# Performance work log

Hardware: AMD Instinct MI355X
Metric: run time of the kernel (lower is better)

Reference implementation:

```python
import jax, jax.numpy as jnp
import numpy as np

# Multi-scale feature pyramid (static: determines per-level slice bounds)
SPATIAL_SHAPES = np.array([[100, 100], [50, 50], [25, 25], [13, 13], [7, 7]])  # (H, W) per level
LEVEL_START = np.concatenate([[0], np.cumsum(SPATIAL_SHAPES[:, 0] * SPATIAL_SHAPES[:, 1])])[:-1]
C = 256       # hidden_inplanes
HEADS = 8     # head_nums
POINTS = 4    # point_nums
LEVELS = 5    # feature_level_nums
FF = 2048     # feedforward_planes
DH = C // HEADS


def setup_inputs() -> dict:
    key = jax.random.key(0)
    ks = jax.random.split(key, 16)
    B = 2
    L = int((SPATIAL_SHAPES[:, 0] * SPATIAL_SHAPES[:, 1]).sum())  # 13343 tokens
    s = 0.02
    return {
        'src': jax.random.normal(ks[0], (B, L, C), jnp.float32),
        'pos': jax.random.normal(ks[1], (B, L, C), jnp.float32) * 0.1,
        'reference_points': jax.random.uniform(ks[2], (B, L, LEVELS, 2), jnp.float32),
        'wv': jax.random.normal(ks[3], (C, C), jnp.float32) * s,
        'bv': jnp.zeros((C,), jnp.float32),
        'wo': jax.random.normal(ks[4], (C, HEADS * LEVELS * POINTS * 2), jnp.float32) * s,
        'bo': jax.random.normal(ks[5], (HEADS * LEVELS * POINTS * 2,), jnp.float32) * 0.5,
        'wa': jax.random.normal(ks[6], (C, HEADS * LEVELS * POINTS), jnp.float32) * s,
        'ba': jnp.zeros((HEADS * LEVELS * POINTS,), jnp.float32),
        'wout': jax.random.normal(ks[7], (C, C), jnp.float32) * s,
        'bout': jnp.zeros((C,), jnp.float32),
        'ln1g': jnp.ones((C,), jnp.float32),
        'ln1b': jnp.zeros((C,), jnp.float32),
        'w1': jax.random.normal(ks[8], (C, FF), jnp.float32) * s,
        'b1': jnp.zeros((FF,), jnp.float32),
        'w2': jax.random.normal(ks[9], (FF, C), jnp.float32) * s,
        'b2': jnp.zeros((C,), jnp.float32),
        'ln2g': jnp.ones((C,), jnp.float32),
        'ln2b': jnp.zeros((C,), jnp.float32),
    }


def layernorm(x, g, b, eps=1e-5):
    m = jnp.mean(x, -1, keepdims=True)
    v = jnp.var(x, -1, keepdims=True)
    return (x - m) * jax.lax.rsqrt(v + eps) * g + b


def bilinear_sample(val, loc, Hs, Ws):
    # val: [B, heads, H*W, dh]   loc: [B, heads, Lq, P, 2] normalized coords in [0,1]
    # grid_sample semantics, align_corners=False, zero padding outside
    px = loc[..., 0] * Ws - 0.5
    py = loc[..., 1] * Hs - 0.5
    x0 = jnp.floor(px); y0 = jnp.floor(py)
    lx = px - x0;       ly = py - y0
    x0i = x0.astype(jnp.int32); y0i = y0.astype(jnp.int32)
    gather = jax.vmap(jax.vmap(lambda v, i: v[i]))  # over batch, head dims
    out = jnp.zeros(loc.shape[:-1] + (val.shape[-1],), val.dtype)
    for dx, dy, w in ((0, 0, (1 - lx) * (1 - ly)), (1, 0, lx * (1 - ly)),
                      (0, 1, (1 - lx) * ly), (1, 1, lx * ly)):
        xi = x0i + dx; yi = y0i + dy
        valid = (xi >= 0) & (xi < Ws) & (yi >= 0) & (yi < Hs)
        idx = jnp.clip(yi, 0, Hs - 1) * Ws + jnp.clip(xi, 0, Ws - 1)
        g = gather(val, idx)  # [B, heads, Lq, P, dh]
        out = out + (w * valid)[..., None] * g
    return out


def msdeform_attn(query, value_in, ref, wv, bv, wo, bo, wa, ba, wout, bout):
    B, Lq, _ = query.shape
    # value projection -> [B, heads, Len, dh]
    value = (value_in @ wv + bv).reshape(B, -1, HEADS, DH).transpose(0, 2, 1, 3)
    offsets = (query @ wo + bo).reshape(B, Lq, HEADS, LEVELS, POINTS, 2)
    attn = jax.nn.softmax((query @ wa + ba).reshape(B, Lq, HEADS, LEVELS * POINTS), -1)
    attn = attn.reshape(B, Lq, HEADS, LEVELS, POINTS)
    # offset normalizer = (W, H) per level
    norml = jnp.asarray(SPATIAL_SHAPES[:, ::-1].copy(), jnp.float32)
    loc = ref[:, :, None, :, None, :] + offsets / norml[None, None, None, :, None, :]
    acc = jnp.zeros((B, Lq, HEADS, DH), query.dtype)
    for l in range(LEVELS):
        Hs, Ws = int(SPATIAL_SHAPES[l, 0]), int(SPATIAL_SHAPES[l, 1])
        s = int(LEVEL_START[l])
        vl = value[:, :, s:s + Hs * Ws, :]
        locl = jnp.transpose(loc[:, :, :, l], (0, 2, 1, 3, 4))  # [B, heads, Lq, P, 2]
        samp = bilinear_sample(vl, locl, Hs, Ws)                 # [B, heads, Lq, P, dh]
        acc = acc + jnp.einsum('bhqpd,bqhp->bqhd', samp, attn[:, :, :, l])
    return acc.reshape(B, Lq, C) @ wout + bout


def reference(src, pos, reference_points, wv, bv, wo, bo, wa, ba, wout, bout,
              ln1g, ln1b, w1, b1, w2, b2, ln2g, ln2b):
    # DeformableTransformerEncoderLayer (eval mode, dropout off)
    q = src + pos
    src2 = msdeform_attn(q, src, reference_points, wv, bv, wo, bo, wa, ba, wout, bout)
    x = layernorm(src + src2, ln1g, ln1b)
    ffn = jax.nn.relu(x @ w1 + b1) @ w2 + b2
    return layernorm(x + ffn, ln2g, ln2b)
```

## Files before the change

kernel.cpp:

```cpp
#include <hip/hip_runtime.h>
#include <hip/hip_bf16.h>
#include <hip/hip_fp16.h>

typedef __hip_bfloat16 bf16;
typedef unsigned short ushort_t;
typedef __attribute__((ext_vector_type(8))) short bf16x8;
typedef __attribute__((ext_vector_type(16))) float f32x16;

__device__ __forceinline__ float us2f(unsigned short u) {
    unsigned int x = ((unsigned int)u) << 16;
    return __uint_as_float(x);
}
__device__ __forceinline__ ushort_t f2us(float f) {
    return ((__hip_bfloat16_raw)__float2bfloat16(f)).x;
}

__device__ __forceinline__ void gl_lds16(const ushort_t* g, ushort_t* l) {
    __builtin_amdgcn_global_load_lds(
        (const __attribute__((address_space(1))) void*)g,
        (__attribute__((address_space(3))) void*)l, 16, 0, 0);
}

__global__ __launch_bounds__(256) void cast2_kernel(
    const float* __restrict__ src, const float* __restrict__ pos,
    bf16* __restrict__ src_b, bf16* __restrict__ q_b, int n)
{
    int i = (blockIdx.x * 256 + threadIdx.x) * 4;
    if (i < n) {
        const float4 s4 = *reinterpret_cast<const float4*>(&src[i]);
        const float4 p4 = *reinterpret_cast<const float4*>(&pos[i]);
        int2 sp, qp;
        sp.x = (unsigned)f2us(s4.x) | ((unsigned)f2us(s4.y) << 16);
        sp.y = (unsigned)f2us(s4.z) | ((unsigned)f2us(s4.w) << 16);
        qp.x = (unsigned)f2us(s4.x + p4.x) | ((unsigned)f2us(s4.y + p4.y) << 16);
        qp.y = (unsigned)f2us(s4.z + p4.z) | ((unsigned)f2us(s4.w + p4.w) << 16);
        *reinterpret_cast<int2*>((ushort_t*)src_b + i) = sp;
        *reinterpret_cast<int2*>((ushort_t*)q_b + i) = qp;
    }
}

__global__ __launch_bounds__(256) void prep_kernel(
    const float* __restrict__ wv, const float* __restrict__ wo,
    const float* __restrict__ wa, const float* __restrict__ wout,
    const float* __restrict__ w1, const float* __restrict__ w2,
    const float* __restrict__ bo, const float* __restrict__ ba,
    bf16* __restrict__ wvt, bf16* __restrict__ wcat, bf16* __restrict__ woutt,
    ushort_t* __restrict__ w1p, ushort_t* __restrict__ w2p,
    float* __restrict__ bcat)
{
    __shared__ float tile[32][33];
    const int b = blockIdx.x;
    const float* W; bf16* Wt = nullptr; ushort_t* Wp = nullptr;
    int K, N, tb, mode = 0;
    if (b < 64)        { W = wv;   Wt = wvt;            K = 256;  N = 256;  tb = b; }
    else if (b < 144)  { W = wo;   Wt = wcat;           K = 256;  N = 320;  tb = b - 64; }
    else if (b < 184)  { W = wa;   Wt = wcat + 320*256; K = 256;  N = 160;  tb = b - 144; }
    else if (b < 248)  { W = wout; Wt = woutt;          K = 256;  N = 256;  tb = b - 184; }
    else if (b < 760)  { W = w1;   Wp = w1p; mode = 1;  K = 256;  N = 2048; tb = b - 248; }
    else if (b < 1272) { W = w2;   Wp = w2p; mode = 2;  K = 2048; N = 256;  tb = b - 760; }
    else {
        int i = (b - 1272) * 256 + threadIdx.x;
        if (i < 320) bcat[i] = bo[i];
        else if (i < 480) bcat[i] = ba[i - 320];
        return;
    }
    const int ntn = N >> 5;
    const int nb = (tb % ntn) * 32, kb = (tb / ntn) * 32;
    const int tx = threadIdx.x & 31, ty = threadIdx.x >> 5;
    #pragma unroll
    for (int i = 0; i < 32; i += 8) {
        int k = kb + ty + i, n = nb + tx;
        tile[ty + i][tx] = (k < K && n < N) ? W[(size_t)k * N + n] : 0.f;
    }
    __syncthreads();
    if (mode == 0) {
        #pragma unroll
        for (int i = 0; i < 32; i += 8) {
            int n = nb + ty + i, k = kb + tx;
            if (n < N && k < K)
                Wt[(size_t)n * K + k] = __float2bfloat16(tile[tx][ty + i]);
        }
    } else if (threadIdx.x < 128) {
        const int l = threadIdx.x & 63, kw = threadIdx.x >> 6;
        const int kb8 = kw * 16 + (l >> 5) * 8;
        const int nx = l & 31;
        ushort_t tmp[8];
        #pragma unroll
        for (int e = 0; e < 8; ++e) tmp[e] = f2us(tile[kb8 + e][nx]);
        size_t base;
        if (mode == 1)
            base = ((size_t)(((nb >> 5) * 8 + (kb >> 5)) * 2 + kw)) * 512;
        else
            base = ((size_t)((((kb >> 7) * 8 + (nb >> 5)) * 4 + ((kb >> 5) & 3)) * 2 + kw)) * 512;
        *reinterpret_cast<int4*>(Wp + base + l * 8) =
            *reinterpret_cast<const int4*>(tmp);
    }
}

template<bool RELU, bool OUT_BF16, bool HAS_RESID, bool RESID_BF16, int NT, int WPE>
__global__ __launch_bounds__(256, WPE) void gemm_mfma_s(
    const ushort_t* __restrict__ A,
    const ushort_t* __restrict__ Bt,
    const float* __restrict__ bias,
    const void* __restrict__ residv,
    void* __restrict__ outv, int M, int N, int K, int mtiles)
{
    __shared__ __align__(16) char smemraw[24576];
    ushort_t* Asmem = (ushort_t*)smemraw;
    ushort_t* Bsmem = (ushort_t*)(smemraw + 4096);
    float (*epi)[68] = (float(*)[68])smemraw;

    const int lid = blockIdx.x;
    const int tbk = lid >> 3;
    const int xb = tbk & (NT - 1);
    const int yg = (tbk / NT) * 8 + (lid & 7);
    if (yg >= mtiles) return;
    const int m0 = yg * 64;
    const int n0 = xb * 128;

    const int tid = threadIdx.x;
    const int lane = tid & 63;
    const int wave = tid >> 6;
    const int l32 = lane & 31;
    const int hi  = lane >> 5;
    const int wm = wave >> 1;
    const int wn = wave & 1;

    const int lsup = lane >> 3;
    const int clin = lane & 7;

    const int gsA = wave * 8 + lsup;
    const int csA = clin ^ (gsA & 7);
    int rA = m0 + gsA * 2 + (csA >> 2); if (rA > M - 1) rA = M - 1;
    const ushort_t* aP = A + (size_t)rA * K + (csA & 3) * 8;
    ushort_t* aL = Asmem + wave * 512;

    const ushort_t* bP[2]; ushort_t* bL[2];
    #pragma unroll
    for (int i = 0; i < 2; ++i) {
        const int gsB = wave * 16 + i * 8 + lsup;
        const int csB = clin ^ (gsB & 7);
        int rB = n0 + gsB * 2 + (csB >> 2); if (rB > N - 1) rB = N - 1;
        bP[i] = Bt + (size_t)rB * K + (csB & 3) * 8;
        bL[i] = Bsmem + (wave * 16 + i * 8) * 64;
    }

    const int arow = wm * 32 + l32;
    const int asup = arow >> 1;
    const ushort_t* aR[2];
    #pragma unroll
    for (int kw = 0; kw < 2; ++kw) {
        const int q = kw * 2 + hi;
        const int slot = (((arow & 1) << 2) | q) ^ (asup & 7);
        aR[kw] = Asmem + asup * 64 + slot * 8;
    }
    const ushort_t* bR[2][2];
    #pragma unroll
    for (int j = 0; j < 2; ++j) {
        const int brow = wn * 64 + j * 32 + l32;
        const int bsup = brow >> 1;
        #pragma unroll
        for (int kw = 0; kw < 2; ++kw) {
            const int q = kw * 2 + hi;
            const int slot = (((brow & 1) << 2) | q) ^ (bsup & 7);
            bR[j][kw] = Bsmem + bsup * 64 + slot * 8;
        }
    }

    f32x16 acc[2] = {};

    auto stage = [&](int ofs) {
        gl_lds16(aP, aL + ofs);             aP    += 32;
        gl_lds16(bP[0], bL[0] + ofs);       bP[0] += 32;
        gl_lds16(bP[1], bL[1] + ofs);       bP[1] += 32;
    };
    auto compute = [&](int ofs) {
        #pragma unroll
        for (int kw = 0; kw < 2; ++kw) {
            const bf16x8 af = *reinterpret_cast<const bf16x8*>(aR[kw] + ofs);
            #pragma unroll
            for (int j = 0; j < 2; ++j)
                acc[j] = __builtin_amdgcn_mfma_f32_32x32x16_bf16(
                    af, *reinterpret_cast<const bf16x8*>(bR[j][kw] + ofs),
                    acc[j], 0, 0, 0);
        }
    };

    const int ntile = K >> 5;
    stage(0);
    for (int t = 0; t < ntile; t += 2) {
        __syncthreads();
        stage(6144);
        compute(0);
        __syncthreads();
        if (t + 2 < ntile) stage(0);
        compute(6144);
    }
    __syncthreads();

    #pragma unroll
    for (int half = 0; half < 2; ++half) {
        if (wn == half) {
            #pragma unroll
            for (int j = 0; j < 2; ++j) {
                const int coll = j * 32 + l32;
                const int n = n0 + half * 64 + coll;
                const float bv = (n < N) ? bias[n] : 0.f;
                #pragma unroll
                for (int r = 0; r < 16; ++r) {
                    const int row = wm * 32 + hi * 4 + (r & 3) + (r >> 2) * 8;
                    epi[row][coll] = acc[j][r] + bv;
                }
            }
        }
        __syncthreads();
        #pragma unroll
        for (int i = 0; i < 4; ++i) {
            const int idx = i * 256 + tid;
            const int row = idx >> 4;
            const int c4  = idx & 15;
            const int m = m0 + row;
            const int n = n0 + half * 64 + c4 * 4;
            if (m < M && n + 3 < N) {
                float4 v = *reinterpret_cast<const float4*>(&epi[row][c4 * 4]);
                if (HAS_RESID) {
                    if (RESID_BF16) {
                        const int2 rw = *reinterpret_cast<const int2*>(
                            (const ushort_t*)residv + (size_t)m * N + n);
                        v.x += us2f((ushort_t)((unsigned)rw.x & 0xffffu));
                        v.y += us2f((ushort_t)((unsigned)rw.x >> 16));
                        v.z += us2f((ushort_t)((unsigned)rw.y & 0xffffu));
                        v.w += us2f((ushort_t)((unsigned)rw.y >> 16));
                    } else {
                        const float4 r4 = *reinterpret_cast<const float4*>(
                            (const float*)residv + (size_t)m * N + n);
                        v.x += r4.x; v.y += r4.y; v.z += r4.z; v.w += r4.w;
                    }
                }
                if (RELU) {
                    v.x = fmaxf(v.x, 0.f); v.y = fmaxf(v.y, 0.f);
                    v.z = fmaxf(v.z, 0.f); v.w = fmaxf(v.w, 0.f);
                }
                if (OUT_BF16) {
                    int2 pk;
                    pk.x = (unsigned)f2us(v.x) | ((unsigned)f2us(v.y) << 16);
                    pk.y = (unsigned)f2us(v.z) | ((unsigned)f2us(v.w) << 16);
                    *reinterpret_cast<int2*>((ushort_t*)outv + (size_t)m * N + n) = pk;
                } else {
                    *reinterpret_cast<float4*>((float*)outv + (size_t)m * N + n) = v;
                }
            }
        }
        if (half == 0) __syncthreads();
    }
}

template<bool RELU, bool OUT_BF16, bool HAS_RESID, bool RESID_BF16, int NT>
__global__ __launch_bounds__(256, 4) void gemm_mfma_b(
    const ushort_t* __restrict__ A,
    const ushort_t* __restrict__ Bt,
    const float* __restrict__ bias,
    const void* __restrict__ residv,
    void* __restrict__ outv, int M, int N, int K, int mtiles)
{
    __shared__ __align__(16) char smemraw[32768];
    ushort_t* Asmem = (ushort_t*)smemraw;
    ushort_t* Bsmem = (ushort_t*)(smemraw + 8192);
    float (*epi)[68] = (float(*)[68])smemraw;

    const int lid = blockIdx.x;
    const int tbk = lid >> 3;
    const int xb = tbk & (NT - 1);
    const int yg = (tbk / NT) * 8 + (lid & 7);
    if (yg >= mtiles) return;
    const int m0 = yg * 128;
    const int n0 = xb * 128;

    const int tid = threadIdx.x;
    const int lane = tid & 63;
    const int wave = tid >> 6;
    const int l32 = lane & 31;
    const int hi  = lane >> 5;
    const int wm = wave >> 1;
    const int wn = wave & 1;

    const int lsup = lane >> 3;
    const int clin = lane & 7;
    const ushort_t *aP[2], *bP[2];
    ushort_t *aL[2], *bL[2];
    #pragma unroll
    for (int i = 0; i < 2; ++i) {
        const int gs = wave * 16 + i * 8 + lsup;
        const int cs = clin ^ (gs & 7);
        int rA = m0 + gs * 2 + (cs >> 2); if (rA > M - 1) rA = M - 1;
        aP[i] = A + (size_t)rA * K + (cs & 3) * 8;
        aL[i] = Asmem + (wave * 16 + i * 8) * 64;
        int rB = n0 + gs * 2 + (cs >> 2); if (rB > N - 1) rB = N - 1;
        bP[i] = Bt + (size_t)rB * K + (cs & 3) * 8;
        bL[i] = Bsmem + (wave * 16 + i * 8) * 64;
    }

    const ushort_t* aR[2][2];
    const ushort_t* bR[2][2];
    #pragma unroll
    for (int mi = 0; mi < 2; ++mi) {
        const int arow = wm * 64 + mi * 32 + l32;
        const int asup = arow >> 1;
        #pragma unroll
        for (int kw = 0; kw < 2; ++kw) {
            const int q = kw * 2 + hi;
            const int slot = (((arow & 1) << 2) | q) ^ (asup & 7);
            aR[mi][kw] = Asmem + asup * 64 + slot * 8;
        }
    }
    #pragma unroll
    for (int ni = 0; ni < 2; ++ni) {
        const int brow = wn * 64 + ni * 32 + l32;
        const int bsup = brow >> 1;
        #pragma unroll
        for (int kw = 0; kw < 2; ++kw) {
            const int q = kw * 2 + hi;
            const int slot = (((brow & 1) << 2) | q) ^ (bsup & 7);
            bR[ni][kw] = Bsmem + bsup * 64 + slot * 8;
        }
    }

    f32x16 a00 = {}, a01 = {}, a10 = {}, a11 = {};

    auto stage = [&](int ofs) {
        gl_lds16(aP[0], aL[0] + ofs); aP[0] += 32;
        gl_lds16(aP[1], aL[1] + ofs); aP[1] += 32;
        gl_lds16(bP[0], bL[0] + ofs); bP[0] += 32;
        gl_lds16(bP[1], bL[1] + ofs); bP[1] += 32;
    };
    auto compute = [&](int ofs) {
        #pragma unroll
        for (int kw = 0; kw < 2; ++kw) {
            const bf16x8 af0 = *reinterpret_cast<const bf16x8*>(aR[0][kw] + ofs);
            const bf16x8 af1 = *reinterpret_cast<const bf16x8*>(aR[1][kw] + ofs);
            const bf16x8 bf0 = *reinterpret_cast<const bf16x8*>(bR[0][kw] + ofs);
            const bf16x8 bf1 = *reinterpret_cast<const bf16x8*>(bR[1][kw] + ofs);
            a00 = __builtin_amdgcn_mfma_f32_32x32x16_bf16(af0, bf0, a00, 0, 0, 0);
            a01 = __builtin_amdgcn_mfma_f32_32x32x16_bf16(af0, bf1, a01, 0, 0, 0);
            a10 = __builtin_amdgcn_mfma_f32_32x32x16_bf16(af1, bf0, a10, 0, 0, 0);
            a11 = __builtin_amdgcn_mfma_f32_32x32x16_bf16(af1, bf1, a11, 0, 0, 0);
        }
    };

    const int ntile = K >> 5;
    stage(0);
    for (int t = 0; t < ntile; t += 2) {
        __syncthreads();
        stage(8192);
        compute(0);
        __syncthreads();
        if (t + 2 < ntile) stage(0);
        compute(8192);
    }
    __syncthreads();

    #pragma unroll
    for (int qd = 0; qd < 4; ++qd) {
        const int rh = qd >> 1, ch = qd & 1;
        if (qd) __syncthreads();
        if (wm == rh && wn == ch) {
            #pragma unroll
            for (int ni = 0; ni < 2; ++ni) {
                const int col = ni * 32 + l32;
                const int n = n0 + ch * 64 + col;
                const float bv = (n < N) ? bias[n] : 0.f;
                #pragma unroll
                for (int mi = 0; mi < 2; ++mi) {
                    const f32x16& ac = (mi == 0) ? (ni == 0 ? a00 : a01)
                                                 : (ni == 0 ? a10 : a11);
                    #pragma unroll
                    for (int r = 0; r < 16; ++r) {
                        const int row = mi * 32 + hi * 4 + (r & 3) + (r >> 2) * 8;
                        epi[row][col] = ac[r] + bv;
                    }
                }
            }
        }
        __syncthreads();
        #pragma unroll
        for (int i = 0; i < 4; ++i) {
            const int idx = i * 256 + tid;
            const int row = idx >> 4;
            const int c4  = idx & 15;
            const int m = m0 + rh * 64 + row;
            const int n = n0 + ch * 64 + c4 * 4;
            if (m < M && n + 3 < N) {
                float4 v = *reinterpret_cast<const float4*>(&epi[row][c4 * 4]);
                if (HAS_RESID) {
                    if (RESID_BF16) {
                        const int2 rw = *reinterpret_cast<const int2*>(
                            (const ushort_t*)residv + (size_t)m * N + n);
                        v.x += us2f((ushort_t)((unsigned)rw.x & 0xffffu));
                        v.y += us2f((ushort_t)((unsigned)rw.x >> 16));
                        v.z += us2f((ushort_t)((unsigned)rw.y & 0xffffu));
                        v.w += us2f((ushort_t)((unsigned)rw.y >> 16));
                    } else {
                        const float4 r4 = *reinterpret_cast<const float4*>(
                            (const float*)residv + (size_t)m * N + n);
                        v.x += r4.x; v.y += r4.y; v.z += r4.z; v.w += r4.w;
                    }
                }
                if (RELU) {
                    v.x = fmaxf(v.x, 0.f); v.y = fmaxf(v.y, 0.f);
                    v.z = fmaxf(v.z, 0.f); v.w = fmaxf(v.w, 0.f);
                }
                if (OUT_BF16) {
                    int2 pk;
                    pk.x = (unsigned)f2us(v.x) | ((unsigned)f2us(v.y) << 16);
                    pk.y = (unsigned)f2us(v.z) | ((unsigned)f2us(v.w) << 16);
                    *reinterpret_cast<int2*>((ushort_t*)outv + (size_t)m * N + n) = pk;
                } else {
                    *reinterpret_cast<float4*>((float*)outv + (size_t)m * N + n) = v;
                }
            }
        }
    }
}

__global__ __launch_bounds__(256, 3) void ffn_fused2(
    const ushort_t* __restrict__ X,
    const ushort_t* __restrict__ W1p,
    const ushort_t* __restrict__ W2p,
    const float* __restrict__ b1, const float* __restrict__ b2,
    const float* __restrict__ g, const float* __restrict__ beta,
    float* __restrict__ out, int M)
{
    __shared__ __align__(16) char smem[33280];
    ushort_t* Xs = (ushort_t*)smem;
    ushort_t* Hs = (ushort_t*)(smem + 16384);
    float (*epi)[260] = (float(*)[260])smem;

    const int m0 = blockIdx.x * 32;
    const int tid = threadIdx.x;
    const int lane = tid & 63;
    const int wave = tid >> 6;
    const int l32 = lane & 31;
    const int hi  = lane >> 5;

    {
        const int lsup = (wave & 1) * 8 + (lane >> 3);
        const int clin = lane & 7;
        const int cs = clin ^ (lsup & 7);
        int r = m0 + lsup * 2 + (cs >> 2); if (r > M - 1) r = M - 1;
        const ushort_t* xp = X + (size_t)r * 256 + (cs & 3) * 8;
        ushort_t* xl = Xs + (wave & 1) * 512;
        #pragma unroll
        for (int p = 0; p < 4; ++p) {
            const int t = p * 2 + (wave >> 1);
            gl_lds16(xp + t * 32, xl + t * 1024);
        }
    }

    int aOff[2];
    {
        const int sr = l32 >> 1;
        #pragma unroll
        for (int kw = 0; kw < 2; ++kw) {
            const int q = kw * 2 + hi;
            const int slot = (((l32 & 1) << 2) | q) ^ (sr & 7);
            aOff[kw] = sr * 64 + slot * 8;
        }
    }
    int hadr[16];
    #pragma unroll
    for (int r = 0; r < 16; ++r) {
        const int m = (r & 3) + 8 * (r >> 2) + 4 * hi;
        const int slot = (((m & 1) << 2) | (l32 >> 3)) ^ ((m >> 1) & 7);
        hadr[r] = wave * 1024 + (m >> 1) * 64 + slot * 8 + (l32 & 7);
    }

    f32x16 za0 = {}, za1 = {};
    __syncthreads();

    for (int c = 0; c < 16; ++c) {
        f32x16 h0 = {}, h1 = {};
        const int hcg = c * 4 + wave;
        const ushort_t* w1c = W1p + (size_t)hcg * 8192;
        #pragma unroll
        for (int t = 0; t < 8; t += 2) {
            #pragma unroll
            for (int kw = 0; kw < 2; ++kw) {
                const bf16x8 a0 = *reinterpret_cast<const bf16x8*>(
                    Xs + t * 1024 + aOff[kw]);
                const bf16x8 a1 = *reinterpret_cast<const bf16x8*>(
                    Xs + (t + 1) * 1024 + aOff[kw]);
                const bf16x8 b0 = *reinterpret_cast<const bf16x8*>(
                    w1c + (t * 2 + kw) * 512 + lane * 8);
                const bf16x8 b1f = *reinterpret_cast<const bf16x8*>(
                    w1c + ((t + 1) * 2 + kw) * 512 + lane * 8);
                h0 = __builtin_amdgcn_mfma_f32_32x32x16_bf16(a0, b0, h0, 0, 0, 0);
                h1 = __builtin_amdgcn_mfma_f32_32x32x16_bf16(a1, b1f, h1, 0, 0, 0);
            }
        }
        const float bb = b1[hcg * 32 + l32];

        __syncthreads();
        #pragma unroll
        for (int r = 0; r < 16; ++r)
            Hs[hadr[r]] = f2us(fmaxf(h0[r] + h1[r] + bb, 0.f));
        __syncthreads();

        const ushort_t* w2c = W2p + (size_t)c * 32768;
        const int nq0 = wave * 2;
        #pragma unroll
        for (int t = 0; t < 4; ++t) {
            #pragma unroll
            for (int kw = 0; kw < 2; ++kw) {
                const bf16x8 af = *reinterpret_cast<const bf16x8*>(
                    Hs + t * 1024 + aOff[kw]);
                const bf16x8 bf0 = *reinterpret_cast<const bf16x8*>(
                    w2c + ((nq0 * 4 + t) * 2 + kw) * 512 + lane * 8);
                const bf16x8 bf1 = *reinterpret_cast<const bf16x8*>(
                    w2c + (((nq0 + 1) * 4 + t) * 2 + kw) * 512 + lane * 8);
                za0 = __builtin_amdgcn_mfma_f32_32x32x16_bf16(af, bf0, za0, 0, 0, 0);
                za1 = __builtin_amdgcn_mfma_f32_32x32x16_bf16(af, bf1, za1, 0, 0, 0);
            }
        }
    }

    __syncthreads();

    #pragma unroll
    for (int j = 0; j < 2; ++j) {
        const int col = wave * 64 + j * 32 + l32;
        const float bz = b2[col];
        const f32x16& zz = j ? za1 : za0;
        #pragma unroll
        for (int r = 0; r < 16; ++r)
            epi[(r & 3) + 8 * (r >> 2) + 4 * hi][col] = zz[r] + bz;
    }
    __syncthreads();

    const int row = tid >> 3, t8 = tid & 7;
    const int m = m0 + row;
    const int mc = (m < M) ? m : (M - 1);
    const ushort_t* xr = X + (size_t)mc * 256 + t8 * 32;
    float v[32];
    float s = 0.f, ss = 0.f;
    #pragma unroll
    for (int i = 0; i < 8; ++i) {
        const float4 e = *reinterpret_cast<const float4*>(
            &epi[row][t8 * 32 + i * 4]);
        const int2 rb = *reinterpret_cast<const int2*>(xr + i * 4);
        const float f0 = e.x + us2f((ushort_t)((unsigned)rb.x & 0xffffu));
        const float f1 = e.y + us2f((ushort_t)((unsigned)rb.x >> 16));
        const float f2 = e.z + us2f((ushort_t)((unsigned)rb.y & 0xffffu));
        const float f3 = e.w + us2f((ushort_t)((unsigned)rb.y >> 16));
        v[i * 4]     = f0; v[i * 4 + 1] = f1;
        v[i * 4 + 2] = f2; v[i * 4 + 3] = f3;
        s  += f0 + f1 + f2 + f3;
        ss += f0 * f0 + f1 * f1 + f2 * f2 + f3 * f3;
    }
    s += __shfl_xor(s, 1); ss += __shfl_xor(ss, 1);
    s += __shfl_xor(s, 2); ss += __shfl_xor(ss, 2);
    s += __shfl_xor(s, 4); ss += __shfl_xor(ss, 4);
    const float mean = s * (1.f / 256.f);
    const float var = ss * (1.f / 256.f) - mean * mean;
    const float rs = rsqrtf(var + 1e-5f);
    if (m < M) {
        #pragma unroll
        for (int i = 0; i < 8; ++i) {
            const float4 g4 = *reinterpret_cast<const float4*>(
                &g[t8 * 32 + i * 4]);
            const float4 b4 = *reinterpret_cast<const float4*>(
                &beta[t8 * 32 + i * 4]);
            float4 o4;
            o4.x = (v[i * 4]     - mean) * rs * g4.x + b4.x;
            o4.y = (v[i * 4 + 1] - mean) * rs * g4.y + b4.y;
            o4.z = (v[i * 4 + 2] - mean) * rs * g4.z + b4.z;
            o4.w = (v[i * 4 + 3] - mean) * rs * g4.w + b4.w;
            *reinterpret_cast<float4*>(
                &out[(size_t)m * 256 + t8 * 32 + i * 4]) = o4;
        }
    }
}

__global__ __launch_bounds__(256) void msda_kernel_v7(
    const ushort_t* __restrict__ og,
    const float* __restrict__ refp,
    const ushort_t* __restrict__ value,
    bf16* __restrict__ out,
    int M, int L)
{
    const int tid = threadIdx.x;
    const int nb = gridDim.x;
    int wk = blockIdx.x;
    if ((nb & 7) == 0) {
        const int per = nb >> 3;
        wk = (blockIdx.x & 7) * per + (blockIdx.x >> 3);
    }
    const int qbase = wk * 8;

    __shared__ float s_attn[8][160];
    __shared__ int2  s_off[1280];
    __shared__ int2  s_wh[1280];

    for (int i = tid; i < 1280; i += 256) {
        int q = i / 160, j = i - q * 160;
        int qq = qbase + q;
        s_attn[q][j] = (qq < M) ? us2f(og[(size_t)qq * 480 + 320 + j]) : 0.f;
    }
    __syncthreads();

    if (tid < 64) {
        float* a = &s_attn[tid >> 3][(tid & 7) * 20];
        float mx = -1e30f;
        #pragma unroll
        for (int i = 0; i < 20; ++i) mx = fmaxf(mx, a[i]);
        float ssum = 0.f;
        #pragma unroll
        for (int i = 0; i < 20; ++i) {
            float e = __expf(a[i] - mx);
            a[i] = e;
            ssum += e;
        }
        float inv = 1.f / ssum;
        #pragma unroll
        for (int i = 0; i < 20; ++i) a[i] *= inv;
    }
    __syncthreads();

    #pragma unroll
    for (int it = 0; it < 5; ++it) {
        const int t = tid + it * 256;
        const int q  = t / 160;
        const int r  = t - q * 160;
        const int l  = (r - (r / 20) * 20) >> 2;
        const int qq = qbase + q;

        int2 offp = {0, 0};
        __half2 h01 = __floats2half2_rn(0.f, 0.f);
        __half2 h23 = h01;
        if (qq < M) {
            const int Wi = (l == 0) ? 100 : (l == 1) ? 50 : (l == 2) ? 25
                         : (l == 3) ? 13 : 7;
            const int s0 = (l == 0) ? 0 : (l == 1) ? 10000 : (l == 2) ? 12500
                         : (l == 3) ? 13125 : 13294;
            const float Wf = (float)Wi;
            const float ox = us2f(og[(size_t)qq * 480 + r * 2]);
            const float oy = us2f(og[(size_t)qq * 480 + r * 2 + 1]);
            const float2 rf = *reinterpret_cast<const float2*>(
                &refp[(size_t)qq * 10 + l * 2]);
            const float a = s_attn[q][r];

            const float px = fmaf(rf.x, Wf, -0.5f) + ox;
            const float py = fmaf(rf.y, Wf, -0.5f) + oy;
            const float x0f = floorf(px);
            const float y0f = floorf(py);
            const float lx = px - x0f;
            const float ly = py - y0f;
            const int x0 = (int)x0f;
            const int y0 = (int)y0f;

            const float wx0v = (x0 >= 0 && x0 < Wi) ? (1.f - lx) : 0.f;
            const float wx1v = (x0 + 1 >= 0 && x0 + 1 < Wi) ? lx : 0.f;
            const float wy0v = (y0 >= 0 && y0 < Wi) ? (1.f - ly) : 0.f;
            const float wy1v = (y0 + 1 >= 0 && y0 + 1 < Wi) ? ly : 0.f;

            const int c0 = min(max(x0, 0), Wi - 2);
            const int r0 = min(max(y0, 0), Wi - 2);
            const float swx0 = (x0 == c0 ? wx0v : 0.f) + (x0 + 1 == c0 ? wx1v : 0.f);
            const float swx1 = (x0 == c0 + 1 ? wx0v : 0.f) + (x0 + 1 == c0 + 1 ? wx1v : 0.f);
            const float swy0 = (y0 == r0 ? wy0v : 0.f) + (y0 + 1 == r0 ? wy1v : 0.f);
            const float swy1 = (y0 == r0 + 1 ? wy0v : 0.f) + (y0 + 1 == r0 + 1 ? wy1v : 0.f);

            offp.x = (s0 + r0 * Wi + c0) * 512;
            offp.y = offp.x + Wi * 512;
            h01 = __floats2half2_rn(a * swx0 * swy0, a * swx1 * swy0);
            h23 = __floats2half2_rn(a * swx0 * swy1, a * swx1 * swy1);
        }
        s_off[t] = offp;
        union { __half2 h; int i; } c0u, c1u;
        c0u.h = h01; c1u.h = h23;
        int2 wpk; wpk.x = c0u.i; wpk.y = c1u.i;
        s_wh[t] = wpk;
    }
    __syncthreads();

    const int qi  = tid >> 5;
    const int g   = tid & 31;
    const int h   = g >> 2;
    const int sub = g & 3;
    const int bq = qbase + qi;
    if (bq >= M) return;
    const int b = bq / L;

    const char* vb = (const char*)value + (size_t)b * L * 512 + h * 64 + sub * 16;

    float acc[8] = {};
    const int tb = qi * 160 + h * 20;
    #pragma unroll 2
    for (int p = 0; p < 20; ++p) {
        const int2 off = s_off[tb + p];
        const int2 whp = s_wh[tb + p];
        const int4 u00 = *reinterpret_cast<const int4*>(vb + off.x);
        const int4 u10 = *reinterpret_cast<const int4*>(vb + off.x + 512);
        const int4 u01 = *reinterpret_cast<const int4*>(vb + off.y);
        const int4 u11 = *reinterpret_cast<const int4*>(vb + off.y + 512);
        union { int i; __half2 h; } w0u, w1u;
        w0u.i = whp.x; w1u.i = whp.y;
        const float2 w01 = __half22float2(w0u.h);
        const float2 w23 = __half22float2(w1u.h);
        #define ACC4(u, wt)                                                        \
            acc[0] = fmaf(wt, __uint_as_float((unsigned)(u).x << 16), acc[0]);      \
            acc[1] = fmaf(wt, __uint_as_float((unsigned)(u).x & 0xffff0000u), acc[1]); \
            acc[2] = fmaf(wt, __uint_as_float((unsigned)(u).y << 16), acc[2]);      \
            acc[3] = fmaf(wt, __uint_as_float((unsigned)(u).y & 0xffff0000u), acc[3]); \
            acc[4] = fmaf(wt, __uint_as_float((unsigned)(u).z << 16), acc[4]);      \
            acc[5] = fmaf(wt, __uint_as_float((unsigned)(u).z & 0xffff0000u), acc[5]); \
            acc[6] = fmaf(wt, __uint_as_float((unsigned)(u).w << 16), acc[6]);      \
            acc[7] = fmaf(wt, __uint_as_float((unsigned)(u).w & 0xffff0000u), acc[7]);
        ACC4(u00, w01.x)
        ACC4(u10, w01.y)
        ACC4(u01, w23.x)
        ACC4(u11, w23.y)
        #undef ACC4
    }

    ushort_t o[8];
    #pragma unroll
    for (int i = 0; i < 8; ++i) o[i] = f2us(acc[i]);
    int4 pkt;
    pkt.x = (int)o[0] | ((int)o[1] << 16);
    pkt.y = (int)o[2] | ((int)o[3] << 16);
    pkt.z = (int)o[4] | ((int)o[5] << 16);
    pkt.w = (int)o[6] | ((int)o[7] << 16);
    *reinterpret_cast<int4*>((ushort_t*)out + (size_t)bq * 256 + h * 32 + sub * 8) = pkt;
}

template<bool OUT_BF16>
__global__ __launch_bounds__(256) void ln_kernel(
    const ushort_t* __restrict__ yb, const float* __restrict__ g,
    const float* __restrict__ bta, void* __restrict__ outv, int M)
{
    const int wave = threadIdx.x >> 6, lane = threadIdx.x & 63;
    const int row = blockIdx.x * 4 + wave;
    if (row >= M) return;
    const int2 raw = *reinterpret_cast<const int2*>(&yb[(size_t)row * 256 + lane * 4]);
    float v0 = us2f((ushort_t)((unsigned)raw.x & 0xffffu));
    float v1 = us2f((ushort_t)((unsigned)raw.x >> 16));
    float v2 = us2f((ushort_t)((unsigned)raw.y & 0xffffu));
    float v3 = us2f((ushort_t)((unsigned)raw.y >> 16));
    float s  = v0 + v1 + v2 + v3;
    float ss = v0 * v0 + v1 * v1 + v2 * v2 + v3 * v3;
    #pragma unroll
    for (int o = 32; o > 0; o >>= 1) {
        s += __shfl_down(s, o);
        ss += __shfl_down(ss, o);
    }
    s = __shfl(s, 0);
    ss = __shfl(ss, 0);
    const float mean = s * (1.f / 256.f);
    const float var = ss * (1.f / 256.f) - mean * mean;
    const float rs = rsqrtf(var + 1e-5f);
    const float4 g4 = *reinterpret_cast<const float4*>(&g[lane * 4]);
    const float4 b4 = *reinterpret_cast<const float4*>(&bta[lane * 4]);
    float4 o4;
    o4.x = (v0 - mean) * rs * g4.x + b4.x;
    o4.y = (v1 - mean) * rs * g4.y + b4.y;
    o4.z = (v2 - mean) * rs * g4.z + b4.z;
    o4.w = (v3 - mean) * rs * g4.w + b4.w;
    if (OUT_BF16) {
        int2 pk;
        pk.x = (unsigned)f2us(o4.x) | ((unsigned)f2us(o4.y) << 16);
        pk.y = (unsigned)f2us(o4.z) | ((unsigned)f2us(o4.w) << 16);
        *reinterpret_cast<int2*>((ushort_t*)outv + (size_t)row * 256 + lane * 4) = pk;
    } else {
        *reinterpret_cast<float4*>((float*)outv + (size_t)row * 256 + lane * 4) = o4;
    }
}

extern "C" void kernel_launch(void* const* d_in, const int* in_sizes, int n_in,
                              void* d_out, int out_size, void* d_ws, size_t ws_size,
                              hipStream_t stream)
{
    const int B = 2, L = 13343, C = 256;
    const int M = B * L;

    const float* src  = (const float*)d_in[0];
    const float* pos  = (const float*)d_in[1];
    const float* refp = (const float*)d_in[2];
    const float* wv   = (const float*)d_in[3];
    const float* bv   = (const float*)d_in[4];
    const float* wo   = (const float*)d_in[5];
    const float* bo   = (const float*)d_in[6];
    const float* wa   = (const float*)d_in[7];
    const float* ba   = (const float*)d_in[8];
    const float* wout = (const float*)d_in[9];
    const float* bout = (const float*)d_in[10];
    const float* ln1g = (const float*)d_in[11];
    const float* ln1b = (const float*)d_in[12];
    const float* w1   = (const float*)d_in[13];
    const float* b1   = (const float*)d_in[14];
    const float* w2   = (const float*)d_in[15];
    const float* b2   = (const float*)d_in[16];
    const float* ln2g = (const float*)d_in[17];
    const float* ln2b = (const float*)d_in[18];

    char* ws = (char*)d_ws;
    const size_t MB = 1ull << 20;
    bf16*  src_b  = (bf16*)(ws + 0);
    bf16*  q_b    = (bf16*)(ws + 14 * MB);
    bf16*  val_b  = (bf16*)(ws + 28 * MB);
    bf16*  og     = (bf16*)(ws + 42 * MB);
    bf16*  acc_b  = (bf16*)(ws + 95 * MB);
    bf16*  y      = (bf16*)(ws + 110 * MB);
    bf16*  x_b    = (bf16*)(ws + 138 * MB);
    bf16* wvt    = (bf16*)(ws + 152 * MB);
    bf16* wcat   = wvt + 256 * 256;
    bf16* woutt  = wcat + 480 * 256;
    ushort_t* w1p = (ushort_t*)(woutt + 256 * 256);
    ushort_t* w2p = w1p + 2048 * 256;
    float* bcat  = (float*)(w2p + 256 * 2048);
    (void)ws_size; (void)n_in; (void)in_sizes; (void)out_size;

    const int mt64  = (M + 63) / 64;
    const int gm8   = (mt64 + 7) / 8;
    const int mt128 = (M + 127) / 128;
    const int gb8   = (mt128 + 7) / 8;
    const int mt32  = (M + 31) / 32;
    const int lnb   = (M + 3) / 4;

    prep_kernel<<<1274, 256, 0, stream>>>(wv, wo, wa, wout, w1, w2, bo, ba,
                                          wvt, wcat, woutt, w1p, w2p, bcat);

    cast2_kernel<<<(M * C / 4 + 255) / 256, 256, 0, stream>>>(
        src, pos, src_b, q_b, M * C);

    gemm_mfma_s<false, true, false, false, 2, 4><<<gm8 * 16, 256, 0, stream>>>(
        (const ushort_t*)src_b, (const ushort_t*)wvt, bv, nullptr, val_b,
        M, 256, 256, mt64);

    gemm_mfma_b<false, true, false, false, 4><<<gb8 * 32, 256, 0, stream>>>(
        (const ushort_t*)q_b, (const ushort_t*)wcat, bcat, nullptr, og,
        M, 480, 256, mt128);

    msda_kernel_v7<<<(M + 7) / 8, 256, 0, stream>>>(
        (const ushort_t*)og, refp, (const ushort_t*)val_b, acc_b, M, L);

    gemm_mfma_s<false, true, true, false, 2, 4><<<gm8 * 16, 256, 0, stream>>>(
        (const ushort_t*)acc_b, (const ushort_t*)woutt, bout, src, y,
        M, 256, 256, mt64);

    ln_kernel<true><<<lnb, 256, 0, stream>>>(
        (const ushort_t*)y, ln1g, ln1b, x_b, M);

    ffn_fused2<<<mt32, 256, 0, stream>>>(
        (const ushort_t*)x_b, w1p, w2p, b1, b2, ln2g, ln2b,
        (float*)d_out, M);
}
```

Before: 352.6 us.

## Keep FFN hidden tile in registers and split second GEMM over K across waves

The fused FFN kernel now computes the first GEMM transposed (weights as the A operand), so the ReLU'd hidden chunk lands in registers in the layout needed as the A operand of the second GEMM. Lanes exchange halves with a cross-lane shuffle instead of writing the chunk to shared memory. This removes two block barriers and an LDS round trip per chunk. Each wave then accumulates all 8 output column tiles over its own slice of K, and the partial sums are reduced through shared memory in a staggered four-phase epilogue. The cost is 128 accumulator registers per thread, which lowers the occupancy bound from 3 to 2 blocks, plus extra epilogue barriers.

Result: slower. 466.0 us (+32.2%).

```diff
diff --git a/kernel.cpp b/kernel.cpp
--- a/kernel.cpp
+++ b/kernel.cpp
@@ -422,7 +422,7 @@
     }
 }
 
-__global__ __launch_bounds__(256, 3) void ffn_fused2(
+__global__ __launch_bounds__(256, 2) void ffn_fused3(
     const ushort_t* __restrict__ X,
     const ushort_t* __restrict__ W1p,
     const ushort_t* __restrict__ W2p,
@@ -432,7 +432,6 @@
 {
     __shared__ __align__(16) char smem[33280];
     ushort_t* Xs = (ushort_t*)smem;
-    ushort_t* Hs = (ushort_t*)(smem + 16384);
     float (*epi)[260] = (float(*)[260])smem;
 
     const int m0 = blockIdx.x * 32;
@@ -441,6 +440,7 @@
     const int wave = tid >> 6;
     const int l32 = lane & 31;
     const int hi  = lane >> 5;
+    const bool hb = (hi != 0);
 
     {
         const int lsup = (wave & 1) * 8 + (lane >> 3);
@@ -466,15 +466,8 @@
             aOff[kw] = sr * 64 + slot * 8;
         }
     }
-    int hadr[16];
-    #pragma unroll
-    for (int r = 0; r < 16; ++r) {
-        const int m = (r & 3) + 8 * (r >> 2) + 4 * hi;
-        const int slot = (((m & 1) << 2) | (l32 >> 3)) ^ ((m >> 1) & 7);
-        hadr[r] = wave * 1024 + (m >> 1) * 64 + slot * 8 + (l32 & 7);
-    }
-
-    f32x16 za0 = {}, za1 = {};
+
+    f32x16 za[8] = {};
     __syncthreads();
 
     for (int c = 0; c < 16; ++c) {
@@ -485,56 +478,79 @@
         for (int t = 0; t < 8; t += 2) {
             #pragma unroll
             for (int kw = 0; kw < 2; ++kw) {
-                const bf16x8 a0 = *reinterpret_cast<const bf16x8*>(
+                const bf16x8 xa0 = *reinterpret_cast<const bf16x8*>(
                     Xs + t * 1024 + aOff[kw]);
-                const bf16x8 a1 = *reinterpret_cast<const bf16x8*>(
+                const bf16x8 xa1 = *reinterpret_cast<const bf16x8*>(
                     Xs + (t + 1) * 1024 + aOff[kw]);
-                const bf16x8 b0 = *reinterpret_cast<const bf16x8*>(
+                const bf16x8 wA0 = *reinterpret_cast<const bf16x8*>(
                     w1c + (t * 2 + kw) * 512 + lane * 8);
-                const bf16x8 b1f = *reinterpret_cast<const bf16x8*>(
+                const bf16x8 wA1 = *reinterpret_cast<const bf16x8*>(
                     w1c + ((t + 1) * 2 + kw) * 512 + lane * 8);
-                h0 = __builtin_amdgcn_mfma_f32_32x32x16_bf16(a0, b0, h0, 0, 0, 0);
-                h1 = __builtin_amdgcn_mfma_f32_32x32x16_bf16(a1, b1f, h1, 0, 0, 0);
+                h0 = __builtin_amdgcn_mfma_f32_32x32x16_bf16(wA0, xa0, h0, 0, 0, 0);
+                h1 = __builtin_amdgcn_mfma_f32_32x32x16_bf16(wA1, xa1, h1, 0, 0, 0);
             }
         }
-        const float bb = b1[hcg * 32 + l32];
-
+
+        float4 bq[4];
+        #pragma unroll
+        for (int p = 0; p < 4; ++p)
+            bq[p] = *reinterpret_cast<const float4*>(b1 + hcg * 32 + p * 8 + 4 * hi);
+        int pk[8];
+        #pragma unroll
+        for (int i = 0; i < 8; ++i) {
+            const int p = i >> 1;
+            const float bv0 = (i & 1) ? bq[p].z : bq[p].x;
+            const float bv1 = (i & 1) ? bq[p].w : bq[p].y;
+            const float v0 = fmaxf(h0[2 * i]     + h1[2 * i]     + bv0, 0.f);
+            const float v1 = fmaxf(h0[2 * i + 1] + h1[2 * i + 1] + bv1, 0.f);
+            pk[i] = (int)((unsigned)f2us(v0) | ((unsigned)f2us(v1) << 16));
+        }
+        int sw[8];
+        #pragma unroll
+        for (int i = 0; i < 8; ++i) sw[i] = __shfl_xor(pk[i], 32);
+
+        union { int4 i4; bf16x8 v; } uf0, uf1;
+        uf0.i4.x = hb ? sw[2] : pk[0];
+        uf0.i4.y = hb ? sw[3] : pk[1];
+        uf0.i4.z = hb ? pk[2] : sw[0];
+        uf0.i4.w = hb ? pk[3] : sw[1];
+        uf1.i4.x = hb ? sw[6] : pk[4];
+        uf1.i4.y = hb ? sw[7] : pk[5];
+        uf1.i4.z = hb ? pk[6] : sw[4];
+        uf1.i4.w = hb ? pk[7] : sw[5];
+
+        const ushort_t* w2c = W2p + (size_t)c * 32768;
+        #pragma unroll
+        for (int nq = 0; nq < 8; ++nq) {
+            const bf16x8 wb0 = *reinterpret_cast<const bf16x8*>(
+                w2c + ((nq * 4 + wave) * 2 + 0) * 512 + lane * 8);
+            const bf16x8 wb1 = *reinterpret_cast<const bf16x8*>(
+                w2c + ((nq * 4 + wave) * 2 + 1) * 512 + lane * 8);
+            za[nq] = __builtin_amdgcn_mfma_f32_32x32x16_bf16(uf0.v, wb0, za[nq], 0, 0, 0);
+            za[nq] = __builtin_amdgcn_mfma_f32_32x32x16_bf16(uf1.v, wb1, za[nq], 0, 0, 0);
+        }
+    }
+
+    __syncthreads();
+
+    #pragma unroll
+    for (int q = 0; q < 4; ++q) {
+        const int cg = (wave + q) & 3;
+        #pragma unroll
+        for (int nq = 0; nq < 8; ++nq) {
+            if ((nq >> 1) == cg) {
+                const int col = nq * 32 + l32;
+                #pragma unroll
+                for (int r = 0; r < 16; ++r) {
+                    const int row = (r & 3) + 8 * (r >> 2) + 4 * hi;
+                    float v = za[nq][r];
+                    if (q) v += epi[row][col];
+                    epi[row][col] = v;
+                }
+            }
+        }
         __syncthreads();
-        #pragma unroll
-        for (int r = 0; r < 16; ++r)
-            Hs[hadr[r]] = f2us(fmaxf(h0[r] + h1[r] + bb, 0.f));
-        __syncthreads();
-
-        const ushort_t* w2c = W2p + (size_t)c * 32768;
-        const int nq0 = wave * 2;
-        #pragma unroll
-        for (int t = 0; t < 4; ++t) {
-            #pragma unroll
-            for (int kw = 0; kw < 2; ++kw) {
-                const bf16x8 af = *reinterpret_cast<const bf16x8*>(
-                    Hs + t * 1024 + aOff[kw]);
-                const bf16x8 bf0 = *reinterpret_cast<const bf16x8*>(
-                    w2c + ((nq0 * 4 + t) * 2 + kw) * 512 + lane * 8);
-                const bf16x8 bf1 = *reinterpret_cast<const bf16x8*>(
-                    w2c + (((nq0 + 1) * 4 + t) * 2 + kw) * 512 + lane * 8);
-                za0 = __builtin_amdgcn_mfma_f32_32x32x16_bf16(af, bf0, za0, 0, 0, 0);
-                za1 = __builtin_amdgcn_mfma_f32_32x32x16_bf16(af, bf1, za1, 0, 0, 0);
-            }
-        }
-    }
-
-    __syncthreads();
-
-    #pragma unroll
-    for (int j = 0; j < 2; ++j) {
-        const int col = wave * 64 + j * 32 + l32;
-        const float bz = b2[col];
-        const f32x16& zz = j ? za1 : za0;
-        #pragma unroll
-        for (int r = 0; r < 16; ++r)
-            epi[(r & 3) + 8 * (r >> 2) + 4 * hi][col] = zz[r] + bz;
-    }
-    __syncthreads();
+    }
 
     const int row = tid >> 3, t8 = tid & 7;
     const int m = m0 + row;
@@ -546,11 +562,13 @@
     for (int i = 0; i < 8; ++i) {
         const float4 e = *reinterpret_cast<const float4*>(
             &epi[row][t8 * 32 + i * 4]);
+        const float4 bz = *reinterpret_cast<const float4*>(
+            &b2[t8 * 32 + i * 4]);
         const int2 rb = *reinterpret_cast<const int2*>(xr + i * 4);
-        const float f0 = e.x + us2f((ushort_t)((unsigned)rb.x & 0xffffu));
-        const float f1 = e.y + us2f((ushort_t)((unsigned)rb.x >> 16));
-        const float f2 = e.z + us2f((ushort_t)((unsigned)rb.y & 0xffffu));
-        const float f3 = e.w + us2f((ushort_t)((unsigned)rb.y >> 16));
+        const float f0 = e.x + bz.x + us2f((ushort_t)((unsigned)rb.x & 0xffffu));
+        const float f1 = e.y + bz.y + us2f((ushort_t)((unsigned)rb.x >> 16));
+        const float f2 = e.z + bz.z + us2f((ushort_t)((unsigned)rb.y & 0xffffu));
+        const float f3 = e.w + bz.w + us2f((ushort_t)((unsigned)rb.y >> 16));
         v[i * 4]     = f0; v[i * 4 + 1] = f1;
         v[i * 4 + 2] = f2; v[i * 4 + 3] = f3;
         s  += f0 + f1 + f2 + f3;
@@ -850,7 +868,7 @@
     ln_kernel<true><<<lnb, 256, 0, stream>>>(
         (const ushort_t*)y, ln1g, ln1b, x_b, M);
 
-    ffn_fused2<<<mt32, 256, 0, stream>>>(
+    ffn_fused3<<<mt32, 256, 0, stream>>>(
         (const ushort_t*)x_b, w1p, w2p, b1, b2, ln2g, ln2b,
         (float*)d_out, M);
 }
```

## Fuse output projection, residual add and first LayerNorm into one kernel

Applied to the files above, without the earlier changes.

Replaces the separate wout GEMM (which wrote a bf16 intermediate y) and the standalone LayerNorm kernel with a single kernel. Each block computes 32 rows of the projection with MFMA, using the same pre-packed weight layout as the FFN kernel, then adds bias and the fp32 residual and applies LayerNorm in an LDS epilogue. This removes one launch and the write and re-read of the intermediate. In exchange, weight fragments are read straight from global memory for every 32-row block, and the residual is now added in fp32 before rounding.

Result: no change. 355.5 us (+0.8%).

```diff
diff --git a/kernel.cpp b/kernel.cpp
--- a/kernel.cpp
+++ b/kernel.cpp
@@ -44,7 +44,8 @@
     const float* __restrict__ wa, const float* __restrict__ wout,
     const float* __restrict__ w1, const float* __restrict__ w2,
     const float* __restrict__ bo, const float* __restrict__ ba,
-    bf16* __restrict__ wvt, bf16* __restrict__ wcat, bf16* __restrict__ woutt,
+    bf16* __restrict__ wvt, bf16* __restrict__ wcat,
+    ushort_t* __restrict__ woutp,
     ushort_t* __restrict__ w1p, ushort_t* __restrict__ w2p,
     float* __restrict__ bcat)
 {
@@ -55,7 +56,7 @@
     if (b < 64)        { W = wv;   Wt = wvt;            K = 256;  N = 256;  tb = b; }
     else if (b < 144)  { W = wo;   Wt = wcat;           K = 256;  N = 320;  tb = b - 64; }
     else if (b < 184)  { W = wa;   Wt = wcat + 320*256; K = 256;  N = 160;  tb = b - 144; }
-    else if (b < 248)  { W = wout; Wt = woutt;          K = 256;  N = 256;  tb = b - 184; }
+    else if (b < 248)  { W = wout; Wp = woutp; mode = 1; K = 256; N = 256;  tb = b - 184; }
     else if (b < 760)  { W = w1;   Wp = w1p; mode = 1;  K = 256;  N = 2048; tb = b - 248; }
     else if (b < 1272) { W = w2;   Wp = w2p; mode = 2;  K = 2048; N = 256;  tb = b - 760; }
     else {
@@ -422,6 +423,129 @@
     }
 }
 
+__global__ __launch_bounds__(256, 4) void woutln_kernel(
+    const ushort_t* __restrict__ A,
+    const ushort_t* __restrict__ Wp,
+    const float* __restrict__ bias,
+    const float* __restrict__ resid,
+    const float* __restrict__ g, const float* __restrict__ beta,
+    bf16* __restrict__ out, int M)
+{
+    __shared__ __align__(16) char smem[33280];
+    ushort_t* Xs = (ushort_t*)smem;
+    float (*epi)[260] = (float(*)[260])smem;
+
+    const int m0 = blockIdx.x * 32;
+    const int tid = threadIdx.x;
+    const int lane = tid & 63;
+    const int wave = tid >> 6;
+    const int l32 = lane & 31;
+    const int hi  = lane >> 5;
+
+    {
+        const int lsup = (wave & 1) * 8 + (lane >> 3);
+        const int clin = lane & 7;
+        const int cs = clin ^ (lsup & 7);
+        int r = m0 + lsup * 2 + (cs >> 2); if (r > M - 1) r = M - 1;
+        const ushort_t* xp = A + (size_t)r * 256 + (cs & 3) * 8;
+        ushort_t* xl = Xs + (wave & 1) * 512;
+        #pragma unroll
+        for (int p = 0; p < 4; ++p) {
+            const int t = p * 2 + (wave >> 1);
+            gl_lds16(xp + t * 32, xl + t * 1024);
+        }
+    }
+
+    int aOff[2];
+    {
+        const int sr = l32 >> 1;
+        #pragma unroll
+        for (int kw = 0; kw < 2; ++kw) {
+            const int q = kw * 2 + hi;
+            const int slot = (((l32 & 1) << 2) | q) ^ (sr & 7);
+            aOff[kw] = sr * 64 + slot * 8;
+        }
+    }
+
+    f32x16 za0 = {}, za1 = {};
+    __syncthreads();
+
+    const int nq0 = wave * 2;
+    #pragma unroll
+    for (int t = 0; t < 8; ++t) {
+        #pragma unroll
+        for (int kw = 0; kw < 2; ++kw) {
+            const bf16x8 af = *reinterpret_cast<const bf16x8*>(
+                Xs + t * 1024 + aOff[kw]);
+            const bf16x8 b0 = *reinterpret_cast<const bf16x8*>(
+                Wp + ((nq0 * 8 + t) * 2 + kw) * 512 + lane * 8);
+            const bf16x8 b1 = *reinterpret_cast<const bf16x8*>(
+                Wp + (((nq0 + 1) * 8 + t) * 2 + kw) * 512 + lane * 8);
+            za0 = __builtin_amdgcn_mfma_f32_32x32x16_bf16(af, b0, za0, 0, 0, 0);
+            za1 = __builtin_amdgcn_mfma_f32_32x32x16_bf16(af, b1, za1, 0, 0, 0);
+        }
+    }
+
+    __syncthreads();
+
+    #pragma unroll
+    for (int j = 0; j < 2; ++j) {
+        const int col = wave * 64 + j * 32 + l32;
+        const float bz = bias[col];
+        const f32x16& zz = j ? za1 : za0;
+        #pragma unroll
+        for (int r = 0; r < 16; ++r)
+            epi[(r & 3) + 8 * (r >> 2) + 4 * hi][col] = zz[r] + bz;
+    }
+    __syncthreads();
+
+    const int row = tid >> 3, t8 = tid & 7;
+    const int m = m0 + row;
+    const int mc = (m < M) ? m : (M - 1);
+    const float* xr = resid + (size_t)mc * 256 + t8 * 32;
+    float v[32];
+    float s = 0.f, ss = 0.f;
+    #pragma unroll
+    for (int i = 0; i < 8; ++i) {
+        const float4 e = *reinterpret_cast<const float4*>(
+            &epi[row][t8 * 32 + i * 4]);
+        const float4 r4 = *reinterpret_cast<const float4*>(xr + i * 4);
+        const float f0 = e.x + r4.x;
+        const float f1 = e.y + r4.y;
+        const float f2 = e.z + r4.z;
+        const float f3 = e.w + r4.w;
+        v[i * 4]     = f0; v[i * 4 + 1] = f1;
+        v[i * 4 + 2] = f2; v[i * 4 + 3] = f3;
+        s  += f0 + f1 + f2 + f3;
+        ss += f0 * f0 + f1 * f1 + f2 * f2 + f3 * f3;
+    }
+    s += __shfl_xor(s, 1); ss += __shfl_xor(ss, 1);
+    s += __shfl_xor(s, 2); ss += __shfl_xor(ss, 2);
+    s += __shfl_xor(s, 4); ss += __shfl_xor(ss, 4);
+    const float mean = s * (1.f / 256.f);
+    const float var = ss * (1.f / 256.f) - mean * mean;
+    const float rs = rsqrtf(var + 1e-5f);
+    if (m < M) {
+        #pragma unroll
+        for (int i = 0; i < 8; ++i) {
+            const float4 g4 = *reinterpret_cast<const float4*>(
+                &g[t8 * 32 + i * 4]);
+            const float4 b4 = *reinterpret_cast<const float4*>(
+                &beta[t8 * 32 + i * 4]);
+            float4 o4;
+            o4.x = (v[i * 4]     - mean) * rs * g4.x + b4.x;
+            o4.y = (v[i * 4 + 1] - mean) * rs * g4.y + b4.y;
+            o4.z = (v[i * 4 + 2] - mean) * rs * g4.z + b4.z;
+            o4.w = (v[i * 4 + 3] - mean) * rs * g4.w + b4.w;
+            int2 pk;
+            pk.x = (unsigned)f2us(o4.x) | ((unsigned)f2us(o4.y) << 16);
+            pk.y = (unsigned)f2us(o4.z) | ((unsigned)f2us(o4.w) << 16);
+            *reinterpret_cast<int2*>(
+                (ushort_t*)out + (size_t)m * 256 + t8 * 32 + i * 4) = pk;
+        }
+    }
+}
+
 __global__ __launch_bounds__(256, 3) void ffn_fused2(
     const ushort_t* __restrict__ X,
     const ushort_t* __restrict__ W1p,
@@ -733,48 +857,6 @@
     *reinterpret_cast<int4*>((ushort_t*)out + (size_t)bq * 256 + h * 32 + sub * 8) = pkt;
 }
 
-template<bool OUT_BF16>
-__global__ __launch_bounds__(256) void ln_kernel(
-    const ushort_t* __restrict__ yb, const float* __restrict__ g,
-    const float* __restrict__ bta, void* __restrict__ outv, int M)
-{
-    const int wave = threadIdx.x >> 6, lane = threadIdx.x & 63;
-    const int row = blockIdx.x * 4 + wave;
-    if (row >= M) return;
-    const int2 raw = *reinterpret_cast<const int2*>(&yb[(size_t)row * 256 + lane * 4]);
-    float v0 = us2f((ushort_t)((unsigned)raw.x & 0xffffu));
-    float v1 = us2f((ushort_t)((unsigned)raw.x >> 16));
-    float v2 = us2f((ushort_t)((unsigned)raw.y & 0xffffu));
-    float v3 = us2f((ushort_t)((unsigned)raw.y >> 16));
-    float s  = v0 + v1 + v2 + v3;
-    float ss = v0 * v0 + v1 * v1 + v2 * v2 + v3 * v3;
-    #pragma unroll
-    for (int o = 32; o > 0; o >>= 1) {
-        s += __shfl_down(s, o);
-        ss += __shfl_down(ss, o);
-    }
-    s = __shfl(s, 0);
-    ss = __shfl(ss, 0);
-    const float mean = s * (1.f / 256.f);
-    const float var = ss * (1.f / 256.f) - mean * mean;
-    const float rs = rsqrtf(var + 1e-5f);
-    const float4 g4 = *reinterpret_cast<const float4*>(&g[lane * 4]);
-    const float4 b4 = *reinterpret_cast<const float4*>(&bta[lane * 4]);
-    float4 o4;
-    o4.x = (v0 - mean) * rs * g4.x + b4.x;
-    o4.y = (v1 - mean) * rs * g4.y + b4.y;
-    o4.z = (v2 - mean) * rs * g4.z + b4.z;
-    o4.w = (v3 - mean) * rs * g4.w + b4.w;
-    if (OUT_BF16) {
-        int2 pk;
-        pk.x = (unsigned)f2us(o4.x) | ((unsigned)f2us(o4.y) << 16);
-        pk.y = (unsigned)f2us(o4.z) | ((unsigned)f2us(o4.w) << 16);
-        *reinterpret_cast<int2*>((ushort_t*)outv + (size_t)row * 256 + lane * 4) = pk;
-    } else {
-        *reinterpret_cast<float4*>((float*)outv + (size_t)row * 256 + lane * 4) = o4;
-    }
-}
-
 extern "C" void kernel_launch(void* const* d_in, const int* in_sizes, int n_in,
                               void* d_out, int out_size, void* d_ws, size_t ws_size,
                               hipStream_t stream)
@@ -809,12 +891,11 @@
     bf16*  val_b  = (bf16*)(ws + 28 * MB);
     bf16*  og     = (bf16*)(ws + 42 * MB);
     bf16*  acc_b  = (bf16*)(ws + 95 * MB);
-    bf16*  y      = (bf16*)(ws + 110 * MB);
     bf16*  x_b    = (bf16*)(ws + 138 * MB);
     bf16* wvt    = (bf16*)(ws + 152 * MB);
     bf16* wcat   = wvt + 256 * 256;
-    bf16* woutt  = wcat + 480 * 256;
-    ushort_t* w1p = (ushort_t*)(woutt + 256 * 256);
+    ushort_t* woutp = (ushort_t*)(wcat + 480 * 256);
+    ushort_t* w1p = woutp + 256 * 256;
     ushort_t* w2p = w1p + 2048 * 256;
     float* bcat  = (float*)(w2p + 256 * 2048);
     (void)ws_size; (void)n_in; (void)in_sizes; (void)out_size;
@@ -824,10 +905,9 @@
     const int mt128 = (M + 127) / 128;
     const int gb8   = (mt128 + 7) / 8;
     const int mt32  = (M + 31) / 32;
-    const int lnb   = (M + 3) / 4;
 
     prep_kernel<<<1274, 256, 0, stream>>>(wv, wo, wa, wout, w1, w2, bo, ba,
-                                          wvt, wcat, woutt, w1p, w2p, bcat);
+                                          wvt, wcat, woutp, w1p, w2p, bcat);
 
     cast2_kernel<<<(M * C / 4 + 255) / 256, 256, 0, stream>>>(
         src, pos, src_b, q_b, M * C);
@@ -843,12 +923,8 @@
     msda_kernel_v7<<<(M + 7) / 8, 256, 0, stream>>>(
         (const ushort_t*)og, refp, (const ushort_t*)val_b, acc_b, M, L);
 
-    gemm_mfma_s<false, true, true, false, 2, 4><<<gm8 * 16, 256, 0, stream>>>(
-        (const ushort_t*)acc_b, (const ushort_t*)woutt, bout, src, y,
-        M, 256, 256, mt64);
-
-    ln_kernel<true><<<lnb, 256, 0, stream>>>(
-        (const ushort_t*)y, ln1g, ln1b, x_b, M);
+    woutln_kernel<<<mt32, 256, 0, stream>>>(
+        (const ushort_t*)acc_b, woutp, bout, src, ln1g, ln1b, x_b, M);
 
     ffn_fused2<<<mt32, 256, 0, stream>>>(
         (const ushort_t*)x_b, w1p, w2p, b1, b2, ln2g, ln2b,
```
